# Optimization experiments

Hardware: AMD Instinct MI355X
Metric: run time of the kernel (lower is better)

Reference implementation:

```python
import jax, jax.numpy as jnp
import numpy as np

RANK_ALPHA = 1.0
IGNORE_INDEX = -100


def setup_inputs() -> dict:
    key = jax.random.key(0)
    k1, k2 = jax.random.split(key)
    B, S, V = 2, 512, 50257
    logits = jax.random.normal(k1, (B, S, V), dtype=jnp.float32)
    target = jax.random.randint(k2, (B, S), 0, V, dtype=jnp.int32)
    return {"logits": logits, "target": target}


def _negative_targets(target, V, dtype):
    # target: [B,S] int. Build mask [B,S,V]: neg[b,i,v]=1 iff some j<i has
    # target[b,j]==v, target[b,j] != ignore, and v != target[b,i].
    B, S = target.shape
    ntarget = jnp.where(target == IGNORE_INDEX, 0, target + 1)  # shift by 1; 0 = pad slot
    ctx = jnp.broadcast_to(ntarget[:, None, :], (B, S, S))       # [B,i,j] = ntarget[b,j]
    tril = jnp.tril(jnp.ones((S, S), dtype=bool), -1)            # strictly lower: j < i
    ctx = jnp.where(tril[None, :, :], ctx, 0)
    ctx = jnp.where(ctx == ntarget[:, :, None], 0, ctx)          # drop cands equal to current target
    neg = jnp.zeros((B, S, V + 1), dtype=dtype)
    b_idx = jnp.arange(B)[:, None, None]
    i_idx = jnp.arange(S)[None, :, None]
    neg = neg.at[b_idx, i_idx, ctx].set(1.0)                     # scatter ones (dup indices ok)
    return neg[..., 1:]                                          # drop pad slot


def reference(logits, target):
    lprobs = jax.nn.log_softmax(logits, axis=-1)                 # [B,S,V]
    V = lprobs.shape[-1]
    neg = jax.lax.stop_gradient(_negative_targets(target, V, lprobs.dtype))

    valid = target != IGNORE_INDEX                               # [B,S]
    tgt = jnp.where(valid, target, 0)
    nll = -jnp.take_along_axis(lprobs, tgt[..., None].astype(jnp.int32), axis=-1)[..., 0]
    mle_loss = jnp.sum(jnp.where(valid, nll, jnp.zeros_like(nll)))

    one_minus_probs = jnp.clip(1.0 - jnp.exp(lprobs), 1e-5, None)
    custom_loss = jnp.sum(-jnp.log(one_minus_probs) * neg)

    weight = jnp.sum(valid).astype(lprobs.dtype)
    loss = (mle_loss + RANK_ALPHA * custom_loss) / weight
    return loss
```

## Files before the change

### kernel.cpp

```cpp
#include <hip/hip_runtime.h>

#define BDIM 512
#define SDIM 512
#define VDIM 50257
#define IGN  (-100)

__device__ __forceinline__ float block_reduce(float v, float* s_red, int t) {
#pragma unroll
    for (int o = 32; o > 0; o >>= 1) v += __shfl_down(v, o, 64);
    int wave = t >> 6;
    int lane = t & 63;
    if (lane == 0) s_red[wave] = v;
    __syncthreads();
    float tot = 0.f;
    if (t == 0) {
#pragma unroll
        for (int w = 0; w < BDIM / 64; ++w) tot += s_red[w];
    }
    __syncthreads();
    return tot;
}

__device__ __forceinline__ float exp4_sum(float4 x) {
    return __expf(x.x) + __expf(x.y) + __expf(x.z) + __expf(x.w);
}

__global__ __launch_bounds__(BDIM) void row_kernel(const float* __restrict__ logits,
                                                   const int* __restrict__ target,
                                                   float* __restrict__ partials) {
    const int r = blockIdx.x;
    const int b = r >> 9;
    const int i = r & (SDIM - 1);
    const float* __restrict__ row = logits + (size_t)r * VDIM;
    const int t = threadIdx.x;

    __shared__ int  s_tgt[SDIM];
    __shared__ unsigned char s_first[SDIM];
    __shared__ float s_red[BDIM / 64];
    __shared__ float s_lse;

    const int* __restrict__ tg = target + b * SDIM;
    for (int j = t; j < SDIM; j += BDIM) s_tgt[j] = tg[j];
    __syncthreads();

    for (int j = t; j < i; j += BDIM) {
        int v = s_tgt[j];
        bool dup = false;
        if (v != IGN) {
            const int4* p4 = (const int4*)s_tgt;
            int k = 0;
#pragma unroll 4
            for (; k + 4 <= j; k += 4) {
                int4 c = p4[k >> 2];
                dup = dup | (c.x == v) | (c.y == v) | (c.z == v) | (c.w == v);
            }
            for (; k < j; ++k) dup = dup | (s_tgt[k] == v);
        }
        s_first[j] = (unsigned char)((v != IGN) && !dup);
    }

    float s0 = 0.f, s1 = 0.f;
    const int mis  = (int)(((size_t)r * VDIM) & 3);
    const int head = (4 - mis) & 3;
    if (t < head) s0 += __expf(row[t]);
    const float4* __restrict__ row4 = (const float4*)(row + head);
    const int nv4 = (VDIM - head) >> 2;
    int v = t;
    for (; v + BDIM < nv4; v += 2 * BDIM) {
        float4 a = row4[v];
        float4 c = row4[v + BDIM];
        s0 += exp4_sum(a);
        s1 += exp4_sum(c);
    }
    if (v < nv4) s0 += exp4_sum(row4[v]);
    const int tail0 = head + (nv4 << 2);
    if (tail0 + t < VDIM) s1 += __expf(row[tail0 + t]);

    float tot = block_reduce(s0 + s1, s_red, t);
    if (t == 0) s_lse = __logf(tot);
    __syncthreads();
    const float lse = s_lse;

    float acc = 0.f;
    const int ti = s_tgt[i];
    for (int j = t; j < i; j += BDIM) {
        if (s_first[j]) {
            int vv = s_tgt[j];
            if (vv != ti) {
                float lp = row[vv] - lse;
                float p  = __expf(lp);
                float om = 1.0f - p;
                om = fmaxf(om, 1e-5f);
                acc -= __logf(om);
            }
        }
    }
    if (t == 0 && ti != IGN) {
        acc -= (row[ti] - lse);
    }

    float row_total = block_reduce(acc, s_red, t);
    if (t == 0) partials[r] = row_total;
}

__global__ __launch_bounds__(1024) void finalize_kernel(const float* __restrict__ partials,
                                                        const int* __restrict__ target,
                                                        float* __restrict__ out) {
    const int t = threadIdx.x;
    float v = partials[t];
    float w = (target[t] != IGN) ? 1.f : 0.f;
#pragma unroll
    for (int o = 32; o > 0; o >>= 1) {
        v += __shfl_down(v, o, 64);
        w += __shfl_down(w, o, 64);
    }
    __shared__ float sv[16], sw[16];
    int wave = t >> 6, lane = t & 63;
    if (lane == 0) { sv[wave] = v; sw[wave] = w; }
    __syncthreads();
    if (t == 0) {
        float tv = 0.f, tw = 0.f;
#pragma unroll
        for (int i = 0; i < 16; ++i) { tv += sv[i]; tw += sw[i]; }
        out[0] = tv / tw;
    }
}

extern "C" void kernel_launch(void* const* d_in, const int* in_sizes, int n_in,
                              void* d_out, int out_size, void* d_ws, size_t ws_size,
                              hipStream_t stream) {
    const float* logits = (const float*)d_in[0];
    const int*   target = (const int*)d_in[1];
    float* out = (float*)d_out;
    float* partials = (float*)d_ws;

    const int rows = in_sizes[1];
    row_kernel<<<rows, BDIM, 0, stream>>>(logits, target, partials);
    finalize_kernel<<<1, 1024, 0, stream>>>(partials, target, out);
}
```

Measured before the change: 289.8 us.

## Fuse finalize into row kernel via atomic ticket and prefetch gathered logits

Removes the separate finalize kernel: each block writes its partial, takes an atomic ticket, and the last block to finish does the global reduction and division. The gathered negative-candidate logits and the target logit are now loaded once per thread before the exp-sum pass, which removes the shared first-occurrence flag array and the second loop. This adds a hipMemsetAsync on the ticket and a fence and atomic per block. Since BDIM equals SDIM, each thread handles exactly one candidate position.

```diff
diff --git a/kernel.cpp b/kernel.cpp
--- a/kernel.cpp
+++ b/kernel.cpp
@@ -4,12 +4,13 @@
 #define SDIM 512
 #define VDIM 50257
 #define IGN  (-100)
+#define NROWS 1024
 
 __device__ __forceinline__ float block_reduce(float v, float* s_red, int t) {
 #pragma unroll
     for (int o = 32; o > 0; o >>= 1) v += __shfl_down(v, o, 64);
-    int wave = t >> 6;
-    int lane = t & 63;
+    const int wave = t >> 6;
+    const int lane = t & 63;
     if (lane == 0) s_red[wave] = v;
     __syncthreads();
     float tot = 0.f;
@@ -27,37 +28,49 @@
 
 __global__ __launch_bounds__(BDIM) void row_kernel(const float* __restrict__ logits,
                                                    const int* __restrict__ target,
-                                                   float* __restrict__ partials) {
+                                                   float* __restrict__ partials,
+                                                   unsigned int* __restrict__ ticket,
+                                                   float* __restrict__ out) {
     const int r = blockIdx.x;
     const int b = r >> 9;
     const int i = r & (SDIM - 1);
     const float* __restrict__ row = logits + (size_t)r * VDIM;
     const int t = threadIdx.x;
 
-    __shared__ int  s_tgt[SDIM];
-    __shared__ unsigned char s_first[SDIM];
+    __shared__ int   s_tgt[SDIM];
     __shared__ float s_red[BDIM / 64];
+    __shared__ float s_w[BDIM / 64];
     __shared__ float s_lse;
+    __shared__ int   s_last;
 
     const int* __restrict__ tg = target + b * SDIM;
     for (int j = t; j < SDIM; j += BDIM) s_tgt[j] = tg[j];
     __syncthreads();
 
-    for (int j = t; j < i; j += BDIM) {
-        int v = s_tgt[j];
-        bool dup = false;
-        if (v != IGN) {
+    const int ti = s_tgt[i];
+
+    bool has = false;
+    int  vv  = 0;
+    if (t < i) {
+        vv = s_tgt[t];
+        if (vv != IGN && vv != ti) {
+            bool dup = false;
             const int4* p4 = (const int4*)s_tgt;
             int k = 0;
 #pragma unroll 4
-            for (; k + 4 <= j; k += 4) {
+            for (; k + 4 <= t; k += 4) {
                 int4 c = p4[k >> 2];
-                dup = dup | (c.x == v) | (c.y == v) | (c.z == v) | (c.w == v);
+                dup = dup | (c.x == vv) | (c.y == vv) | (c.z == vv) | (c.w == vv);
             }
-            for (; k < j; ++k) dup = dup | (s_tgt[k] == v);
+            for (; k < t; ++k) dup = dup | (s_tgt[k] == vv);
+            has = !dup;
         }
-        s_first[j] = (unsigned char)((v != IGN) && !dup);
     }
+
+    float pv = 0.f;
+    if (has) pv = row[vv];
+    float rti = 0.f;
+    if (t == 0 && ti != IGN) rti = row[ti];
 
     float s0 = 0.f, s1 = 0.f;
     const int mis  = (int)(((size_t)r * VDIM) & 3);
@@ -82,47 +95,42 @@
     const float lse = s_lse;
 
     float acc = 0.f;
-    const int ti = s_tgt[i];
-    for (int j = t; j < i; j += BDIM) {
-        if (s_first[j]) {
-            int vv = s_tgt[j];
-            if (vv != ti) {
-                float lp = row[vv] - lse;
-                float p  = __expf(lp);
-                float om = 1.0f - p;
-                om = fmaxf(om, 1e-5f);
-                acc -= __logf(om);
-            }
-        }
+    if (has) {
+        float p  = __expf(pv - lse);
+        float om = fmaxf(1.0f - p, 1e-5f);
+        acc -= __logf(om);
     }
-    if (t == 0 && ti != IGN) {
-        acc -= (row[ti] - lse);
-    }
+    if (t == 0 && ti != IGN) acc -= (rti - lse);
 
     float row_total = block_reduce(acc, s_red, t);
-    if (t == 0) partials[r] = row_total;
-}
 
-__global__ __launch_bounds__(1024) void finalize_kernel(const float* __restrict__ partials,
-                                                        const int* __restrict__ target,
-                                                        float* __restrict__ out) {
-    const int t = threadIdx.x;
-    float v = partials[t];
-    float w = (target[t] != IGN) ? 1.f : 0.f;
+    if (t == 0) {
+        partials[r] = row_total;
+        __threadfence();
+        unsigned int old = atomicAdd(ticket, 1u);
+        s_last = ((old & (NROWS - 1u)) == (NROWS - 1u)) ? 1 : 0;
+    }
+    __syncthreads();
+    if (s_last) {
+        __threadfence();
+        float fv = partials[t] + partials[t + BDIM];
+        float fw = ((target[t] != IGN) ? 1.f : 0.f) +
+                   ((target[t + BDIM] != IGN) ? 1.f : 0.f);
 #pragma unroll
-    for (int o = 32; o > 0; o >>= 1) {
-        v += __shfl_down(v, o, 64);
-        w += __shfl_down(w, o, 64);
-    }
-    __shared__ float sv[16], sw[16];
-    int wave = t >> 6, lane = t & 63;
-    if (lane == 0) { sv[wave] = v; sw[wave] = w; }
-    __syncthreads();
-    if (t == 0) {
-        float tv = 0.f, tw = 0.f;
+        for (int o = 32; o > 0; o >>= 1) {
+            fv += __shfl_down(fv, o, 64);
+            fw += __shfl_down(fw, o, 64);
+        }
+        const int wave = t >> 6;
+        const int lane = t & 63;
+        if (lane == 0) { s_red[wave] = fv; s_w[wave] = fw; }
+        __syncthreads();
+        if (t == 0) {
+            float tv = 0.f, tw = 0.f;
 #pragma unroll
-        for (int i = 0; i < 16; ++i) { tv += sv[i]; tw += sw[i]; }
-        out[0] = tv / tw;
+            for (int q = 0; q < BDIM / 64; ++q) { tv += s_red[q]; tw += s_w[q]; }
+            out[0] = tv / tw;
+        }
     }
 }
 
@@ -133,8 +141,8 @@
     const int*   target = (const int*)d_in[1];
     float* out = (float*)d_out;
     float* partials = (float*)d_ws;
+    unsigned int* ticket = (unsigned int*)((char*)d_ws + NROWS * sizeof(float));
 
-    const int rows = in_sizes[1];
-    row_kernel<<<rows, BDIM, 0, stream>>>(logits, target, partials);
-    finalize_kernel<<<1, 1024, 0, stream>>>(partials, target, out);
+    hipMemsetAsync(ticket, 0, sizeof(unsigned int), stream);
+    row_kernel<<<NROWS, BDIM, 0, stream>>>(logits, target, partials, ticket, out);
 }
```

Result: slower. 331.3 us (+14.3%).
